# Kernel tuning notes

Hardware: AMD Instinct MI355X
Metric: run time of the kernel (lower is better)

## Reference

```python
import jax, jax.numpy as jnp
import numpy as np

N, E, D, H = 100000, 1600000, 128, 128


def setup_inputs() -> dict:
    key = jax.random.key(0)
    ks = jax.random.split(key, 7)
    x = jax.random.normal(ks[0], (N, D), dtype=jnp.float32)
    edge_index = jax.random.randint(ks[1], (2, E), 0, N, dtype=jnp.int64)
    edge_weight = jax.random.uniform(ks[2], (E,), dtype=jnp.float32)
    s = 1.0 / np.sqrt(D)
    W0 = jax.random.normal(ks[3], (D, H), dtype=jnp.float32) * s
    b0 = jnp.zeros((H,), dtype=jnp.float32)
    W1 = jax.random.normal(ks[4], (H, H), dtype=jnp.float32) * (1.0 / np.sqrt(H))
    b1 = jnp.zeros((H,), dtype=jnp.float32)
    return {"x": x, "edge_weight": edge_weight, "W0": W0, "b0": b0,
            "W1": W1, "b1": b1, "edge_index": edge_index}


def reference(x, edge_weight, W0, b0, W1, b1, edge_index):
    src, dst = edge_index[0], edge_index[1]
    n = x.shape[0]
    # gcn_norm with self-loops (fill_value=1): deg includes the self-loop weight
    deg = jax.ops.segment_sum(edge_weight, dst, num_segments=n) + 1.0  # [N]
    dis = jnp.where(deg > 0, jax.lax.rsqrt(deg), 0.0)                  # deg^-1/2
    norm = dis[src] * edge_weight * dis[dst]                           # [E]
    self_coef = dis * dis                                              # self-loop norm = 1/deg

    def gcn_layer(h, W, b):
        hW = h @ W                                                     # [N,H]
        agg = jax.ops.segment_sum(norm[:, None] * hW[src], dst, num_segments=n)
        agg = agg + self_coef[:, None] * hW                            # self-loop term
        return jax.nn.relu(agg + b)

    h1 = gcn_layer(x, W0, b0)
    h2 = gcn_layer(h1, W1, b1)
    return jnp.concatenate([h1, h2], axis=1)  # [N, 2H]
```

## Files before the change

### kernel.cpp

```cpp
#include <hip/hip_runtime.h>
#include <hip/hip_fp16.h>


typedef unsigned long long u64;
typedef _Float16 f16;
typedef f16 f16x4 __attribute__((ext_vector_type(4)));
typedef f16 f16x8 __attribute__((ext_vector_type(8)));
typedef float f32x4 __attribute__((ext_vector_type(4)));

__global__ __launch_bounds__(256) void k_init(u64* degcnt, int n) {
    int i = blockIdx.x * 256 + threadIdx.x;
    if (i < n) degcnt[i] = (u64)(1u << 24);
}

__global__ __launch_bounds__(256) void k_wfrag(const float* __restrict__ W0,
                                               const float* __restrict__ W1,
                                               __half* __restrict__ Wf) {
    int idx = blockIdx.x * 256 + threadIdx.x;
    const float* W = (idx < 2048) ? W0 : W1;
    int id = idx & 2047;
    int l = id & 63, nt = (id >> 6) & 7, ks = id >> 9;
    int n = nt * 16 + (l & 15);
    int kb = ks * 32 + ((l >> 4) & 3) * 4;
    union { int4 v; __half h[8]; } pk;
#pragma unroll
    for (int j = 0; j < 8; ++j) {
        int k = kb + (j & 3) + 16 * (j >> 2);
        pk.h[j] = __float2half(W[k * 128 + n]);
    }
    *(int4*)(Wf + (size_t)idx * 8) = pk.v;
}

__global__ __launch_bounds__(256) void k_dis(const u64* __restrict__ degcnt,
                                             float* dis, int* cursor, int n) {
    int i = blockIdx.x * 256 + threadIdx.x;
    if (i < n) {
        u64 v = degcnt[i];
        float deg = (float)(unsigned)(v & 0xffffffffull) * (1.0f / 16777216.0f);
        dis[i] = rsqrtf(deg);
        cursor[i] = (int)(v >> 32);
    }
}

__global__ __launch_bounds__(256) void k_scan1(int* data, int* sums, int n) {
    __shared__ int tmp[256];
    int gid = blockIdx.x * 256 + threadIdx.x;
    int v = (gid < n) ? data[gid] : 0;
    tmp[threadIdx.x] = v;
    __syncthreads();
    for (int off = 1; off < 256; off <<= 1) {
        int t = (threadIdx.x >= off) ? tmp[threadIdx.x - off] : 0;
        __syncthreads();
        tmp[threadIdx.x] += t;
        __syncthreads();
    }
    if (gid < n) data[gid] = tmp[threadIdx.x] - v;
    if (threadIdx.x == 255) sums[blockIdx.x] = tmp[255];
}

__global__ __launch_bounds__(512) void k_scan2(int* sums, int nb) {
    __shared__ int tmp[512];
    int v = (threadIdx.x < nb) ? sums[threadIdx.x] : 0;
    tmp[threadIdx.x] = v;
    __syncthreads();
    for (int off = 1; off < 512; off <<= 1) {
        int t = (threadIdx.x >= off) ? tmp[threadIdx.x - off] : 0;
        __syncthreads();
        tmp[threadIdx.x] += t;
        __syncthreads();
    }
    if (threadIdx.x < nb) sums[threadIdx.x] = tmp[threadIdx.x] - v;
}

__global__ __launch_bounds__(256) void k_scan3(int* data, const int* sums, int n) {
    int gid = blockIdx.x * 256 + threadIdx.x;
    if (gid < n) data[gid] += sums[blockIdx.x];
}

__global__ __launch_bounds__(256) void k_scatter(const int* __restrict__ src,
                                                 const int* __restrict__ dst,
                                                 const float* __restrict__ ew,
                                                 const unsigned short* __restrict__ rank,
                                                 const float* __restrict__ dis,
                                                 const int* __restrict__ rowstart,
                                                 int2* ep, int e) {
    int i0 = blockIdx.x * 2048 + threadIdx.x;
#pragma unroll
    for (int u = 0; u < 8; ++u) {
        int i = i0 + u * 256;
        if (i < e) {
            int s = src[i], d = dst[i];
            float nm = dis[s] * ew[i] * dis[d];
            int pos = rowstart[d] + (int)rank[i];
            ep[pos] = make_int2(s, __float_as_int(nm));
        }
    }
}

__device__ __forceinline__ void gemm_body(const float* __restrict__ A, int lda,
                                          const __half* __restrict__ Wf,
                                          __half* __restrict__ C, int n,
                                          int bid, int t, f16* AF) {
    const int row0 = bid * 64;
    {
        const int r = t >> 2, q = t & 3;
        const int gr = row0 + r;
        float4 v[8];
        if (gr < n) {
            const float4* ap = (const float4*)(A + (size_t)gr * lda + q * 32);
#pragma unroll
            for (int u = 0; u < 8; ++u) v[u] = ap[u];
        } else {
#pragma unroll
            for (int u = 0; u < 8; ++u) v[u] = make_float4(0.f, 0.f, 0.f, 0.f);
        }
        const int w = r >> 4, rr = r & 15;
#pragma unroll
        for (int u = 0; u < 8; ++u) {
            const int s = u & 3, g = u >> 2;
            f16x4 hv;
            hv[0] = (f16)v[u].x; hv[1] = (f16)v[u].y;
            hv[2] = (f16)v[u].z; hv[3] = (f16)v[u].w;
            const int off = ((w * 4 + q) * 64 + rr + 16 * s) * 8 + g * 4;
            *(f16x4*)&AF[off] = hv;
        }
    }
    __syncthreads();

    const int w2 = t >> 6, l = t & 63;
    f32x4 acc[8];
#pragma unroll
    for (int i = 0; i < 8; ++i) acc[i] = (f32x4){0.f, 0.f, 0.f, 0.f};

#pragma unroll
    for (int ks = 0; ks < 4; ++ks) {
        f16x8 af = *(f16x8*)&AF[((w2 * 4 + ks) * 64 + l) * 8];
#pragma unroll
        for (int nt = 0; nt < 8; ++nt) {
            f16x8 wf = *(const f16x8*)(Wf + ((size_t)(ks * 8 + nt) * 64 + l) * 8);
            acc[nt] = __builtin_amdgcn_mfma_f32_16x16x32_f16(wf, af, acc[nt], 0, 0, 0);
        }
    }

    const int node = row0 + w2 * 16 + (l & 15);
    if (node < n) {
        const int c0 = ((l >> 4) & 3) * 4;
#pragma unroll
        for (int nt = 0; nt < 8; ++nt) {
            union { short4 s4; __half h[4]; } pk;
#pragma unroll
            for (int r2 = 0; r2 < 4; ++r2) pk.h[r2] = __float2half(acc[nt][r2]);
            *(short4*)(C + (size_t)node * 128 + nt * 16 + c0) = pk.s4;
        }
    }
}

__global__ __launch_bounds__(256) void k_hist_gemm(
        u64* __restrict__ degcnt, const float* __restrict__ ew,
        const int* __restrict__ dst, unsigned short* __restrict__ rank,
        int e, int gH,
        const float* __restrict__ A, int lda, const __half* __restrict__ Wf,
        __half* __restrict__ C, int n) {
    __shared__ f16 AF[8192];
    const int bid = blockIdx.x;
    if (bid < gH) {
        int i0 = bid * 2048 + threadIdx.x;
#pragma unroll
        for (int u = 0; u < 8; ++u) {
            int i = i0 + u * 256;
            if (i < e) {
                unsigned fx = (unsigned)(ew[i] * 16777216.0f + 0.5f);
                u64 old = atomicAdd(&degcnt[dst[i]], ((u64)1 << 32) | (u64)fx);
                rank[i] = (unsigned short)(old >> 32);
            }
        }
    } else {
        gemm_body(A, lda, Wf, C, n, bid - gH, threadIdx.x, AF);
    }
}

__global__ __launch_bounds__(256) void k_gemm(const float* __restrict__ A, int lda,
                                              const __half* __restrict__ Wf,
                                              __half* __restrict__ C, int n) {
    __shared__ f16 AF[8192];
    gemm_body(A, lda, Wf, C, n, blockIdx.x, threadIdx.x, AF);
}

__global__ __launch_bounds__(256) void k_agg(const __half* __restrict__ hW,
                                             const int2* __restrict__ ep,
                                             const int* __restrict__ rowstart,
                                             const float* __restrict__ dis,
                                             const float* __restrict__ bias,
                                             float* __restrict__ outcol,
                                             int n, int e) {
    int wid = blockIdx.x * 4 + (threadIdx.x >> 6);
    int lane = threadIdx.x & 63;
    if (wid >= n) return;

    int start = rowstart[wid];
    int end   = (wid == n - 1) ? e : rowstart[wid + 1];
    start = __builtin_amdgcn_readfirstlane(start);
    end   = __builtin_amdgcn_readfirstlane(end);

    float di = dis[wid];
    float2 h = __half22float2(*(const __half2*)(hW + (size_t)wid * 128 + lane * 2));
    float2 acc;
    acc.x = di * di * h.x;
    acc.y = di * di * h.y;

    int j = start;
    for (; j + 7 < end; j += 8) {
        int2 r[8];
        __half2 v[8];
#pragma unroll
        for (int u = 0; u < 8; ++u) r[u] = ep[j + u];
#pragma unroll
        for (int u = 0; u < 8; ++u)
            v[u] = *(const __half2*)(hW + (size_t)r[u].x * 128 + lane * 2);
#pragma unroll
        for (int u = 0; u < 8; ++u) {
            float nm = __int_as_float(r[u].y);
            float2 f = __half22float2(v[u]);
            acc.x += nm * f.x;
            acc.y += nm * f.y;
        }
    }
    for (; j < end; ++j) {
        int2 rec = ep[j];
        float nm = __int_as_float(rec.y);
        float2 v = __half22float2(*(const __half2*)(hW + (size_t)rec.x * 128 + lane * 2));
        acc.x += nm * v.x;
        acc.y += nm * v.y;
    }

    float2 b = *(const float2*)(bias + lane * 2);
    float2 o;
    o.x = fmaxf(acc.x + b.x, 0.f);
    o.y = fmaxf(acc.y + b.y, 0.f);
    *(float2*)(outcol + (size_t)wid * 256 + lane * 2) = o;
}

extern "C" void kernel_launch(void* const* d_in, const int* in_sizes, int n_in,
                              void* d_out, int out_size, void* d_ws, size_t ws_size,
                              hipStream_t stream) {
    const float* x  = (const float*)d_in[0];
    const float* ew = (const float*)d_in[1];
    const float* W0 = (const float*)d_in[2];
    const float* b0 = (const float*)d_in[3];
    const float* W1 = (const float*)d_in[4];
    const float* b1 = (const float*)d_in[5];
    const int*   ei = (const int*)d_in[6];

    const int N = in_sizes[0] / 128;
    const int E = in_sizes[1];
    const int* src = ei;
    const int* dst = ei + E;
    float* out = (float*)d_out;

    u64*   degcnt = (u64*)d_ws;
    float* dis    = (float*)(degcnt + N);
    int*   cursor = (int*)(dis + N);
    int2*  ep     = (int2*)(cursor + N);
    __half* hW    = (__half*)(ep + E);
    unsigned short* rank = (unsigned short*)((float*)hW + (size_t)N * 64);
    __half* Wf    = (__half*)((float*)hW + (size_t)N * 64 + (size_t)(E + 1) / 2);
    int*   sums   = (int*)((float*)Wf + 16384);

    const int gN = (N + 255) / 256;
    const int gH = (E + 2047) / 2048;
    const int gG = (N + 63) / 64;
    const int gA = (N + 3) / 4;
    const int nb = gN;

    k_wfrag<<<16, 256, 0, stream>>>(W0, W1, Wf);
    k_init<<<gN, 256, 0, stream>>>(degcnt, N);
    k_hist_gemm<<<gH + gG, 256, 0, stream>>>(degcnt, ew, dst, rank, E, gH,
                                             x, 128, Wf, hW, N);
    k_dis<<<gN, 256, 0, stream>>>(degcnt, dis, cursor, N);
    k_scan1<<<nb, 256, 0, stream>>>(cursor, sums, N);
    k_scan2<<<1, 512, 0, stream>>>(sums, nb);
    k_scan3<<<nb, 256, 0, stream>>>(cursor, sums, N);
    k_scatter<<<gH, 256, 0, stream>>>(src, dst, ew, rank, dis, cursor, ep, E);

    k_agg<<<gA, 256, 0, stream>>>(hW, ep, cursor, dis, b0, out, N, E);

    k_gemm<<<gG, 256, 0, stream>>>(out, 256, Wf + 16384, hW, N);
    k_agg<<<gA, 256, 0, stream>>>(hW, ep, cursor, dis, b1, out + 128, N, E);
}
```

Baseline: 298.7 us.

## Fuse setup kernels, load GEMM A directly to registers, unroll aggregation deeper

Merges k_init and k_wfrag into one launch and folds the k_dis degree/rsqrt step into the first scan kernel, cutting two launches. The GEMM body now loads A fragments straight from global memory into MFMA registers, dropping the LDS staging and the barrier. The histogram part is capped at 256 blocks that loop over edge chunks, so more of the grid goes to GEMM blocks. The aggregation loop gains 16-wide and 4-wide unrolled stages to keep more gathers in flight. Risks include uncoalesced per-lane A loads and more register use in k_agg, which may lower occupancy.

```diff
diff --git a/kernel.cpp b/kernel.cpp
--- a/kernel.cpp
+++ b/kernel.cpp
@@ -4,48 +4,128 @@
 
 typedef unsigned long long u64;
 typedef _Float16 f16;
-typedef f16 f16x4 __attribute__((ext_vector_type(4)));
 typedef f16 f16x8 __attribute__((ext_vector_type(8)));
 typedef float f32x4 __attribute__((ext_vector_type(4)));
 
-__global__ __launch_bounds__(256) void k_init(u64* degcnt, int n) {
-    int i = blockIdx.x * 256 + threadIdx.x;
-    if (i < n) degcnt[i] = (u64)(1u << 24);
-}
-
-__global__ __launch_bounds__(256) void k_wfrag(const float* __restrict__ W0,
+__global__ __launch_bounds__(256) void k_setup(u64* degcnt, int n, int gN,
+                                               const float* __restrict__ W0,
                                                const float* __restrict__ W1,
                                                __half* __restrict__ Wf) {
-    int idx = blockIdx.x * 256 + threadIdx.x;
-    const float* W = (idx < 2048) ? W0 : W1;
-    int id = idx & 2047;
-    int l = id & 63, nt = (id >> 6) & 7, ks = id >> 9;
-    int n = nt * 16 + (l & 15);
-    int kb = ks * 32 + ((l >> 4) & 3) * 4;
-    union { int4 v; __half h[8]; } pk;
-#pragma unroll
-    for (int j = 0; j < 8; ++j) {
-        int k = kb + (j & 3) + 16 * (j >> 2);
-        pk.h[j] = __float2half(W[k * 128 + n]);
-    }
-    *(int4*)(Wf + (size_t)idx * 8) = pk.v;
-}
-
-__global__ __launch_bounds__(256) void k_dis(const u64* __restrict__ degcnt,
-                                             float* dis, int* cursor, int n) {
-    int i = blockIdx.x * 256 + threadIdx.x;
-    if (i < n) {
-        u64 v = degcnt[i];
-        float deg = (float)(unsigned)(v & 0xffffffffull) * (1.0f / 16777216.0f);
-        dis[i] = rsqrtf(deg);
-        cursor[i] = (int)(v >> 32);
-    }
-}
-
-__global__ __launch_bounds__(256) void k_scan1(int* data, int* sums, int n) {
+    int bid = blockIdx.x;
+    if (bid < gN) {
+        int i = bid * 256 + threadIdx.x;
+        if (i < n) degcnt[i] = (u64)(1u << 24);
+    } else {
+        int idx = (bid - gN) * 256 + threadIdx.x;
+        const float* W = (idx < 2048) ? W0 : W1;
+        int id = idx & 2047;
+        int l = id & 63, nt = (id >> 6) & 7, ks = id >> 9;
+        int nn = nt * 16 + (l & 15);
+        int kb = ks * 32 + ((l >> 4) & 3) * 4;
+        union { int4 v; __half h[8]; } pk;
+#pragma unroll
+        for (int j = 0; j < 8; ++j) {
+            int k = kb + (j & 3) + 16 * (j >> 2);
+            pk.h[j] = __float2half(W[k * 128 + nn]);
+        }
+        *(int4*)(Wf + (size_t)idx * 8) = pk.v;
+    }
+}
+
+__device__ __forceinline__ void gemm_body(const float* __restrict__ A, int lda,
+                                          const __half* __restrict__ Wf,
+                                          __half* __restrict__ C, int n,
+                                          int bid, int t) {
+    const int w2 = t >> 6, l = t & 63;
+    const int node = bid * 64 + w2 * 16 + (l & 15);
+    const int koff = ((l >> 4) & 3) * 4;
+    const bool ok = node < n;
+    const float* ap = A + (size_t)(ok ? node : 0) * lda;
+
+    f16x8 af[4];
+#pragma unroll
+    for (int ks = 0; ks < 4; ++ks) {
+        float4 a0 = make_float4(0.f, 0.f, 0.f, 0.f), a1 = a0;
+        if (ok) {
+            a0 = *(const float4*)(ap + ks * 32 + koff);
+            a1 = *(const float4*)(ap + ks * 32 + koff + 16);
+        }
+        f16x8 h;
+        h[0] = (f16)a0.x; h[1] = (f16)a0.y; h[2] = (f16)a0.z; h[3] = (f16)a0.w;
+        h[4] = (f16)a1.x; h[5] = (f16)a1.y; h[6] = (f16)a1.z; h[7] = (f16)a1.w;
+        af[ks] = h;
+    }
+
+    f32x4 acc[8];
+#pragma unroll
+    for (int i = 0; i < 8; ++i) acc[i] = (f32x4){0.f, 0.f, 0.f, 0.f};
+
+#pragma unroll
+    for (int ks = 0; ks < 4; ++ks) {
+#pragma unroll
+        for (int nt = 0; nt < 8; ++nt) {
+            f16x8 wf = *(const f16x8*)(Wf + ((size_t)(ks * 8 + nt) * 64 + l) * 8);
+            acc[nt] = __builtin_amdgcn_mfma_f32_16x16x32_f16(wf, af[ks], acc[nt], 0, 0, 0);
+        }
+    }
+
+    if (ok) {
+        const int c0 = ((l >> 4) & 3) * 4;
+#pragma unroll
+        for (int nt = 0; nt < 8; ++nt) {
+            union { short4 s4; __half h[4]; } pk;
+#pragma unroll
+            for (int r2 = 0; r2 < 4; ++r2) pk.h[r2] = __float2half(acc[nt][r2]);
+            *(short4*)(C + (size_t)node * 128 + nt * 16 + c0) = pk.s4;
+        }
+    }
+}
+
+__global__ __launch_bounds__(256) void k_hist_gemm(
+        u64* __restrict__ degcnt, const float* __restrict__ ew,
+        const int* __restrict__ dst, unsigned short* __restrict__ rank,
+        int e, int gH,
+        const float* __restrict__ A, int lda, const __half* __restrict__ Wf,
+        __half* __restrict__ C, int n) {
+    const int bid = blockIdx.x;
+    if (bid < gH) {
+        const int nch = (e + 2047) >> 11;
+        for (int c = bid; c < nch; c += gH) {
+            int i0 = c * 2048 + threadIdx.x;
+#pragma unroll
+            for (int u = 0; u < 8; ++u) {
+                int i = i0 + u * 256;
+                if (i < e) {
+                    unsigned fx = (unsigned)(ew[i] * 16777216.0f + 0.5f);
+                    u64 old = atomicAdd(&degcnt[dst[i]], ((u64)1 << 32) | (u64)fx);
+                    rank[i] = (unsigned short)(old >> 32);
+                }
+            }
+        }
+    } else {
+        gemm_body(A, lda, Wf, C, n, bid - gH, threadIdx.x);
+    }
+}
+
+__global__ __launch_bounds__(256) void k_gemm(const float* __restrict__ A, int lda,
+                                              const __half* __restrict__ Wf,
+                                              __half* __restrict__ C, int n) {
+    gemm_body(A, lda, Wf, C, n, blockIdx.x, threadIdx.x);
+}
+
+__global__ __launch_bounds__(256) void k_scan1(const u64* __restrict__ degcnt,
+                                               float* __restrict__ dis,
+                                               int* __restrict__ data,
+                                               int* __restrict__ sums, int n) {
     __shared__ int tmp[256];
     int gid = blockIdx.x * 256 + threadIdx.x;
-    int v = (gid < n) ? data[gid] : 0;
+    int v = 0;
+    if (gid < n) {
+        u64 dc = degcnt[gid];
+        float deg = (float)(unsigned)(dc & 0xffffffffull) * (1.0f / 16777216.0f);
+        dis[gid] = rsqrtf(deg);
+        v = (int)(dc >> 32);
+    }
     tmp[threadIdx.x] = v;
     __syncthreads();
     for (int off = 1; off < 256; off <<= 1) {
@@ -97,95 +177,6 @@
     }
 }
 
-__device__ __forceinline__ void gemm_body(const float* __restrict__ A, int lda,
-                                          const __half* __restrict__ Wf,
-                                          __half* __restrict__ C, int n,
-                                          int bid, int t, f16* AF) {
-    const int row0 = bid * 64;
-    {
-        const int r = t >> 2, q = t & 3;
-        const int gr = row0 + r;
-        float4 v[8];
-        if (gr < n) {
-            const float4* ap = (const float4*)(A + (size_t)gr * lda + q * 32);
-#pragma unroll
-            for (int u = 0; u < 8; ++u) v[u] = ap[u];
-        } else {
-#pragma unroll
-            for (int u = 0; u < 8; ++u) v[u] = make_float4(0.f, 0.f, 0.f, 0.f);
-        }
-        const int w = r >> 4, rr = r & 15;
-#pragma unroll
-        for (int u = 0; u < 8; ++u) {
-            const int s = u & 3, g = u >> 2;
-            f16x4 hv;
-            hv[0] = (f16)v[u].x; hv[1] = (f16)v[u].y;
-            hv[2] = (f16)v[u].z; hv[3] = (f16)v[u].w;
-            const int off = ((w * 4 + q) * 64 + rr + 16 * s) * 8 + g * 4;
-            *(f16x4*)&AF[off] = hv;
-        }
-    }
-    __syncthreads();
-
-    const int w2 = t >> 6, l = t & 63;
-    f32x4 acc[8];
-#pragma unroll
-    for (int i = 0; i < 8; ++i) acc[i] = (f32x4){0.f, 0.f, 0.f, 0.f};
-
-#pragma unroll
-    for (int ks = 0; ks < 4; ++ks) {
-        f16x8 af = *(f16x8*)&AF[((w2 * 4 + ks) * 64 + l) * 8];
-#pragma unroll
-        for (int nt = 0; nt < 8; ++nt) {
-            f16x8 wf = *(const f16x8*)(Wf + ((size_t)(ks * 8 + nt) * 64 + l) * 8);
-            acc[nt] = __builtin_amdgcn_mfma_f32_16x16x32_f16(wf, af, acc[nt], 0, 0, 0);
-        }
-    }
-
-    const int node = row0 + w2 * 16 + (l & 15);
-    if (node < n) {
-        const int c0 = ((l >> 4) & 3) * 4;
-#pragma unroll
-        for (int nt = 0; nt < 8; ++nt) {
-            union { short4 s4; __half h[4]; } pk;
-#pragma unroll
-            for (int r2 = 0; r2 < 4; ++r2) pk.h[r2] = __float2half(acc[nt][r2]);
-            *(short4*)(C + (size_t)node * 128 + nt * 16 + c0) = pk.s4;
-        }
-    }
-}
-
-__global__ __launch_bounds__(256) void k_hist_gemm(
-        u64* __restrict__ degcnt, const float* __restrict__ ew,
-        const int* __restrict__ dst, unsigned short* __restrict__ rank,
-        int e, int gH,
-        const float* __restrict__ A, int lda, const __half* __restrict__ Wf,
-        __half* __restrict__ C, int n) {
-    __shared__ f16 AF[8192];
-    const int bid = blockIdx.x;
-    if (bid < gH) {
-        int i0 = bid * 2048 + threadIdx.x;
-#pragma unroll
-        for (int u = 0; u < 8; ++u) {
-            int i = i0 + u * 256;
-            if (i < e) {
-                unsigned fx = (unsigned)(ew[i] * 16777216.0f + 0.5f);
-                u64 old = atomicAdd(&degcnt[dst[i]], ((u64)1 << 32) | (u64)fx);
-                rank[i] = (unsigned short)(old >> 32);
-            }
-        }
-    } else {
-        gemm_body(A, lda, Wf, C, n, bid - gH, threadIdx.x, AF);
-    }
-}
-
-__global__ __launch_bounds__(256) void k_gemm(const float* __restrict__ A, int lda,
-                                              const __half* __restrict__ Wf,
-                                              __half* __restrict__ C, int n) {
-    __shared__ f16 AF[8192];
-    gemm_body(A, lda, Wf, C, n, blockIdx.x, threadIdx.x, AF);
-}
-
 __global__ __launch_bounds__(256) void k_agg(const __half* __restrict__ hW,
                                              const int2* __restrict__ ep,
                                              const int* __restrict__ rowstart,
@@ -209,6 +200,22 @@
     acc.y = di * di * h.y;
 
     int j = start;
+    for (; j + 15 < end; j += 16) {
+        int2 r[16];
+        __half2 v[16];
+#pragma unroll
+        for (int u = 0; u < 16; ++u) r[u] = ep[j + u];
+#pragma unroll
+        for (int u = 0; u < 16; ++u)
+            v[u] = *(const __half2*)(hW + (size_t)r[u].x * 128 + lane * 2);
+#pragma unroll
+        for (int u = 0; u < 16; ++u) {
+            float nm = __int_as_float(r[u].y);
+            float2 f = __half22float2(v[u]);
+            acc.x += nm * f.x;
+            acc.y += nm * f.y;
+        }
+    }
     for (; j + 7 < end; j += 8) {
         int2 r[8];
         __half2 v[8];
@@ -219,6 +226,22 @@
             v[u] = *(const __half2*)(hW + (size_t)r[u].x * 128 + lane * 2);
 #pragma unroll
         for (int u = 0; u < 8; ++u) {
+            float nm = __int_as_float(r[u].y);
+            float2 f = __half22float2(v[u]);
+            acc.x += nm * f.x;
+            acc.y += nm * f.y;
+        }
+    }
+    for (; j + 3 < end; j += 4) {
+        int2 r[4];
+        __half2 v[4];
+#pragma unroll
+        for (int u = 0; u < 4; ++u) r[u] = ep[j + u];
+#pragma unroll
+        for (int u = 0; u < 4; ++u)
+            v[u] = *(const __half2*)(hW + (size_t)r[u].x * 128 + lane * 2);
+#pragma unroll
+        for (int u = 0; u < 4; ++u) {
             float nm = __int_as_float(r[u].y);
             float2 f = __half22float2(v[u]);
             acc.x += nm * f.x;
@@ -267,20 +290,19 @@
     int*   sums   = (int*)((float*)Wf + 16384);
 
     const int gN = (N + 255) / 256;
-    const int gH = (E + 2047) / 2048;
+    const int gH = 256;
+    const int gE8 = (E + 2047) / 2048;
     const int gG = (N + 63) / 64;
     const int gA = (N + 3) / 4;
     const int nb = gN;
 
-    k_wfrag<<<16, 256, 0, stream>>>(W0, W1, Wf);
-    k_init<<<gN, 256, 0, stream>>>(degcnt, N);
+    k_setup<<<gN + 16, 256, 0, stream>>>(degcnt, N, gN, W0, W1, Wf);
     k_hist_gemm<<<gH + gG, 256, 0, stream>>>(degcnt, ew, dst, rank, E, gH,
                                              x, 128, Wf, hW, N);
-    k_dis<<<gN, 256, 0, stream>>>(degcnt, dis, cursor, N);
-    k_scan1<<<nb, 256, 0, stream>>>(cursor, sums, N);
+    k_scan1<<<nb, 256, 0, stream>>>(degcnt, dis, cursor, sums, N);
     k_scan2<<<1, 512, 0, stream>>>(sums, nb);
     k_scan3<<<nb, 256, 0, stream>>>(cursor, sums, N);
-    k_scatter<<<gH, 256, 0, stream>>>(src, dst, ew, rank, dis, cursor, ep, E);
+    k_scatter<<<gE8, 256, 0, stream>>>(src, dst, ew, rank, dis, cursor, ep, E);
 
     k_agg<<<gA, 256, 0, stream>>>(hW, ep, cursor, dis, b0, out, N, E);
 
```

Result: faster. 280.4 us (-6.1%).
